# Performance work log

Hardware: AMD Instinct MI355X
Metric: run time of the kernel (lower is better)

Reference implementation:

```python
import jax, jax.numpy as jnp
import numpy as np

N = 64      # SSM state size (hidden_size)
H = 1024    # channels
L = 2048    # sequence length
BATCH = 8


def setup_inputs() -> dict:
    key = jax.random.key(0)
    ks = jax.random.split(key, 12)
    s = 1.0 / np.sqrt(N)
    n = jnp.arange(N, dtype=jnp.float32)
    return {
        "r": jax.random.normal(ks[0], (BATCH, L, H), dtype=jnp.float32),
        "B_re": jax.random.normal(ks[1], (N,), dtype=jnp.float32) * s,
        "B_im": jax.random.normal(ks[2], (N,), dtype=jnp.float32) * s,
        "C_re": jax.random.normal(ks[3], (H, N), dtype=jnp.float32) * s,
        "C_im": jax.random.normal(ks[4], (H, N), dtype=jnp.float32) * s,
        "P_re": jax.random.normal(ks[5], (N,), dtype=jnp.float32) * s,
        "P_im": jax.random.normal(ks[6], (N,), dtype=jnp.float32) * s,
        "Q_re": jax.random.normal(ks[7], (N,), dtype=jnp.float32) * s,
        "Q_im": jax.random.normal(ks[8], (N,), dtype=jnp.float32) * s,
        # HiPPO-LegS-like diagonal: negative real part for stability, imag ~ pi*n
        "diag_re": -0.5 * jnp.ones((N,), dtype=jnp.float32),
        "diag_im": jnp.pi * (n - N / 2.0),
        "step": jnp.array([1e-3], dtype=jnp.float32),
        "D": jnp.zeros((1,), dtype=jnp.float32),
    }


def _dplr_kernel(Bc, Cc, Pc, Qc, Lam, step, seq_len):
    # Standard S4 DPLR generating function evaluated at roots of unity,
    # then inverse FFT -> real convolution kernel K_c of shape (H, L).
    z = jnp.exp(-2j * jnp.pi * jnp.arange(seq_len) / seq_len).astype(jnp.complex64)  # (L,)
    g = (2.0 / step) * (1.0 - z) / (1.0 + z)                                          # (L,)
    cden = 1.0 / (g[:, None] - Lam[None, :])                                          # (L,N) Cauchy denom
    k00 = jnp.einsum('hn,ln->hl', Cc * Bc, cden)   # (H,L)
    k01 = jnp.einsum('hn,ln->hl', Cc * Pc, cden)   # (H,L)
    k10 = jnp.einsum('n,ln->l', Qc * Bc, cden)     # (L,)
    k11 = jnp.einsum('n,ln->l', Qc * Pc, cden)     # (L,)
    at_roots = (2.0 / (1.0 + z)) * (k00 - k01 * (k10 / (1.0 + k11)))  # (H,L)
    return jnp.fft.ifft(at_roots, axis=-1).real


def reference(r, B_re, B_im, C_re, C_im, P_re, P_im, Q_re, Q_im,
              diag_re, diag_im, step, D):
    step_c = jnp.maximum(step[0], 1e-6)
    Bc = B_re + 1j * B_im
    Cc = C_re + 1j * C_im
    Pc = P_re + 1j * P_im
    Qc = Q_re + 1j * Q_im
    Lam = diag_re + 1j * diag_im
    seq_len = r.shape[1]
    K = _dplr_kernel(Bc, Cc, Pc, Qc, Lam, step_c, seq_len)  # (H, L)
    # causal FFT convolution along the sequence axis
    nfft = 2 * seq_len
    Kf = jnp.fft.rfft(K, n=nfft, axis=-1)            # (H, nfft//2+1)
    uf = jnp.fft.rfft(r, n=nfft, axis=1)             # (B, nfft//2+1, H)
    h1 = jnp.fft.irfft(uf * Kf.T[None], n=nfft, axis=1)[:, :seq_len]  # (B,L,H)
    y1 = h1 + D[0] * r
    return jax.nn.gelu(y1, approximate=False)
```

## Files before the change

kernel.cpp:

```cpp
#include <hip/hip_runtime.h>
#include <math.h>

#define SSM_N 64
#define SSM_H 1024
#define SSM_L 2048
#define SSM_B 8
#define FFTN 2048
#define NT 256
#define NT2 512

#define PSWZ(a) ((a) ^ (((a) >> 4) & 15))

typedef float f2 __attribute__((ext_vector_type(2)));
static __device__ __forceinline__ f2 mkf2(float a, float b){ f2 v; v.x = a; v.y = b; return v; }

static __device__ __forceinline__ f2 cmul(f2 a, f2 b){
  return mkf2(-a.y, a.y) * mkf2(b.y, b.x) + mkf2(a.x, a.x) * b;
}
static __device__ __forceinline__ f2 cconj(f2 a){ return mkf2(a.x, -a.y); }

template<bool INV> static __device__ __forceinline__ f2 mul_mi(f2 a){
  return INV ? mkf2(-a.y, a.x) : mkf2(a.y, -a.x);
}
template<bool INV> static __device__ __forceinline__ f2 mul_w81(f2 a){
  const float r = 0.70710678118654752440f;
  return INV ? (r * mkf2(a.x - a.y, a.y + a.x)) : (r * mkf2(a.x + a.y, a.y - a.x));
}
template<bool INV> static __device__ __forceinline__ f2 mul_w83(f2 a){
  const float r = 0.70710678118654752440f;
  return INV ? (r * mkf2(-(a.x + a.y), a.x - a.y)) : (r * mkf2(a.y - a.x, -(a.x + a.y)));
}

#define W8C0 1.f
#define W8S0 0.f
#define W8C1 0.92387953251f
#define W8S1 (-0.38268343236f)
#define W8C2 0.70710678119f
#define W8S2 (-0.70710678119f)
#define W8C3 0.38268343236f
#define W8S3 (-0.92387953251f)
#define W8C4 0.f
#define W8S4 (-1.f)
#define W8C5 (-0.38268343236f)
#define W8S5 (-0.92387953251f)
#define W8C6 (-0.70710678119f)
#define W8S6 (-0.70710678119f)
#define W8C7 (-0.92387953251f)
#define W8S7 (-0.38268343236f)

template<bool INV>
static __device__ __forceinline__ void bfly8(const f2* x, f2* y)
{
  f2 t0=x[0]+x[4], t4=x[0]-x[4];
  f2 t1=x[1]+x[5], t5=x[1]-x[5];
  f2 t2=x[2]+x[6], t6=x[2]-x[6];
  f2 t3=x[3]+x[7], t7=x[3]-x[7];
  f2 b0=t0+t2, b2=t0-t2, b1=t1+t3, b3=t1-t3;
  f2 mb3 = mul_mi<INV>(b3);
  y[0]=b0+b1; y[4]=b0-b1; y[2]=b2+mb3; y[6]=b2-mb3;
  f2 v1 = mul_w81<INV>(t5), v2 = mul_mi<INV>(t6), v3 = mul_w83<INV>(t7);
  f2 a0=t4+v2, a2=t4-v2, a1=v1+v3, a3=v1-v3;
  f2 ma3 = mul_mi<INV>(a3);
  y[1]=a0+a1; y[5]=a0-a1; y[3]=a2+ma3; y[7]=a2-ma3;
}

template<bool INV>
static __device__ __forceinline__ void calc_w8(const f2* __restrict__ tw, int j, f2* w)
{
  f2 w1 = tw[j];
  if (INV) w1.y = -w1.y;
  w[1]=w1; w[2]=cmul(w1,w1); w[3]=cmul(w[2],w1); w[4]=cmul(w[2],w[2]);
  w[5]=cmul(w[3],w[2]); w[6]=cmul(w[3],w[3]); w[7]=cmul(w[4],w[3]);
}

static __device__ __forceinline__ void twstore(f2* __restrict__ dst, const f2* y, const f2* w,
                                               int base, int S)
{
  dst[PSWZ(base)]     = y[0];
  dst[PSWZ(base+S)]   = cmul(y[1],w[1]);
  dst[PSWZ(base+2*S)] = cmul(y[2],w[2]);
  dst[PSWZ(base+3*S)] = cmul(y[3],w[3]);
  dst[PSWZ(base+4*S)] = cmul(y[4],w[4]);
  dst[PSWZ(base+5*S)] = cmul(y[5],w[5]);
  dst[PSWZ(base+6*S)] = cmul(y[6],w[6]);
  dst[PSWZ(base+7*S)] = cmul(y[7],w[7]);
}

template<bool INV>
static __device__ __forceinline__ void bfly8_store(f2* __restrict__ dst, const f2* __restrict__ tw,
                                                   f2* x, int j, int base, int S)
{
  f2 y[8]; bfly8<INV>(x, y);
  f2 w[8]; calc_w8<INV>(tw, j, w);
  twstore(dst, y, w, base, S);
}

template<bool INV, bool ZTOP>
static __device__ __forceinline__ void stage8_first(const f2* __restrict__ src, f2* __restrict__ dst,
                                                    const f2* __restrict__ tw, int t, int st)
{
  const f2* sp = src + st;
  f2 x[8];
  if (ZTOP) {
    #pragma unroll
    for (int q = 0; q < 4; ++q) { x[q] = sp[256*q]; x[q+4] = mkf2(0.f, 0.f); }
  } else {
    #pragma unroll
    for (int q = 0; q < 8; ++q) x[q] = sp[256*q];
  }
  bfly8_store<INV>(dst, tw, x, t, t*8, 1);
}

template<bool INV, int S>
static __device__ __forceinline__ void stage8_mid(const f2* __restrict__ src, f2* __restrict__ dst,
                                                  const f2* __restrict__ tw, int t, int st)
{
  const f2* sp = src + st;
  f2 x[8];
  #pragma unroll
  for (int q = 0; q < 8; ++q) x[q] = sp[256*q];
  int i = t & (S-1);
  int j = t - i;
  bfly8_store<INV>(dst, tw, x, j, i + j*8, S);
}

template<bool INV, int S>
static __device__ __forceinline__ void stage8_mid_ip(f2* __restrict__ buf, const f2* __restrict__ tw,
                                                     int t, int st)
{
  f2 x[8];
  #pragma unroll
  for (int q = 0; q < 8; ++q) x[q] = buf[st + 256*q];
  __syncthreads();
  int i = t & (S-1);
  int j = t - i;
  bfly8_store<INV>(buf, tw, x, j, i + j*8, S);
  __syncthreads();
}

template<bool INV, bool HALFOUT>
static __device__ __forceinline__ void stage4f(const f2* __restrict__ src, f2* __restrict__ dst, int st)
{
  #pragma unroll
  for (int hh = 0; hh < 2; ++hh) {
    const f2* sp = src + st + 256*hh;
    f2* wp = dst + st + 256*hh;
    f2 x0=sp[0], x1=sp[512], x2=sp[1024], x3=sp[1536];
    f2 a0=x0+x2, a2=x0-x2, a1=x1+x3, a3=x1-x3;
    f2 m = mul_mi<INV>(a3);
    wp[0]   = a0+a1;
    wp[512] = a2+m;
    if (!HALFOUT) {
      wp[1024] = a0-a1;
      wp[1536] = a2-m;
    }
  }
}

template<bool INV>
static __device__ __forceinline__ void stage4f_ip(f2* __restrict__ buf, int st)
{
  f2 xr[2][4];
  #pragma unroll
  for (int hh = 0; hh < 2; ++hh) {
    const f2* sp = buf + st + 256*hh;
    xr[hh][0]=sp[0]; xr[hh][1]=sp[512]; xr[hh][2]=sp[1024]; xr[hh][3]=sp[1536];
  }
  __syncthreads();
  #pragma unroll
  for (int hh = 0; hh < 2; ++hh) {
    f2* wp = buf + st + 256*hh;
    f2 a0=xr[hh][0]+xr[hh][2], a2=xr[hh][0]-xr[hh][2];
    f2 a1=xr[hh][1]+xr[hh][3], a3=xr[hh][1]-xr[hh][3];
    f2 m = mul_mi<INV>(a3);
    wp[0]    = a0+a1;
    wp[512]  = a2+m;
    wp[1024] = a0-a1;
    wp[1536] = a2-m;
  }
  __syncthreads();
}

template<bool INV>
static __device__ __forceinline__ void stage4f_reg(const f2* __restrict__ src, f2* out, int st)
{
  #pragma unroll
  for (int hh = 0; hh < 2; ++hh) {
    const f2* sp = src + st + 256*hh;
    f2 x0=sp[0], x1=sp[512], x2=sp[1024], x3=sp[1536];
    f2 a0=x0+x2, a2=x0-x2, a1=x1+x3, a3=x1-x3;
    f2 m = mul_mi<INV>(a3);
    out[hh]   = a0+a1;
    out[hh+2] = a2+m;
    out[hh+4] = a0-a1;
    out[hh+6] = a2-m;
  }
}

static __device__ __forceinline__ f2 init_tw(f2* tw, int t)
{
  float s, c;
  sincosf(-6.2831853071795864769f * (float)t / (float)FFTN, &s, &c);
  f2 v = mkf2(c, s);
  tw[t] = v;
  return v;
}

__global__ __launch_bounds__(256) void kprep(
    const float* __restrict__ B_re, const float* __restrict__ B_im,
    const float* __restrict__ P_re, const float* __restrict__ P_im,
    const float* __restrict__ Q_re, const float* __restrict__ Q_im,
    const float* __restrict__ diag_re, const float* __restrict__ diag_im,
    const float* __restrict__ step,
    f2* __restrict__ cdenT, f2* __restrict__ f2v, f2* __restrict__ facv)
{
  int gid = blockIdx.x * 256 + threadIdx.x;
  int l = gid >> 3, s = gid & 7;
  double stepc = (double)step[0]; if (stepc < 1e-6) stepc = 1e-6;
  double ang = -2.0 * 3.14159265358979323846 * (double)l / (double)SSM_L;
  double zr = cos(ang), zi = sin(ang);
  double dr = 1.0 + zr, di = zi;
  double nr = 1.0 - zr, ni = -zi;
  double den = dr*dr + di*di;
  double i2s = 2.0 / stepc;
  double gr = i2s * (nr*dr + ni*di) / den;
  double gi = i2s * (ni*dr - nr*di) / den;
  double k10r=0.0, k10i=0.0, k11r=0.0, k11i=0.0;
  #pragma unroll
  for (int q = 0; q < 8; ++q) {
    int n = s*8 + q;
    double ar = gr - (double)diag_re[n];
    double ai = gi - (double)diag_im[n];
    double d2 = ar*ar + ai*ai;
    double cr = ar/d2, ci = -ai/d2;
    cdenT[n*SSM_L + l] = mkf2((float)cr, (float)ci);
    double qr = (double)Q_re[n], qi = (double)Q_im[n];
    double br = (double)B_re[n], bi = (double)B_im[n];
    double pr = (double)P_re[n], pi = (double)P_im[n];
    double qbr = qr*br - qi*bi, qbi = qr*bi + qi*br;
    double qpr = qr*pr - qi*pi, qpi = qr*pi + qi*pr;
    k10r += qbr*cr - qbi*ci; k10i += qbr*ci + qbi*cr;
    k11r += qpr*cr - qpi*ci; k11i += qpr*ci + qpi*cr;
  }
  #pragma unroll
  for (int off = 1; off < 8; off <<= 1) {
    k10r += __shfl_xor(k10r, off);
    k10i += __shfl_xor(k10i, off);
    k11r += __shfl_xor(k11r, off);
    k11i += __shfl_xor(k11i, off);
  }
  if (s == 0) {
    f2v[l] = mkf2((float)(2.0*dr/den), (float)(-2.0*di/den));
    double er = 1.0 + k11r, ei = k11i;
    double ed = er*er + ei*ei;
    facv[l] = mkf2((float)((k10r*er + k10i*ei)/ed), (float)((k10i*er - k10r*ei)/ed));
  }
}

__global__ __launch_bounds__(NT2, 4) void kkern(
    const float* __restrict__ C_re, const float* __restrict__ C_im,
    const float* __restrict__ B_re, const float* __restrict__ B_im,
    const float* __restrict__ P_re, const float* __restrict__ P_im,
    const f2* __restrict__ cdenT, const f2* __restrict__ f2v, const f2* __restrict__ facv,
    float4* __restrict__ PQg)
{
  __shared__ f2 bufA[2][FFTN];
  __shared__ f2 bufB[2][FFTN];
  __shared__ f2 tw[256];
  int t = threadIdx.x;
  int tt = t & 255, ch = t >> 8, stt = PSWZ(tt);
  int h0 = blockIdx.x * 2;
  if (t < 256) init_tw(tw, t);
  f2* cbs = bufA[0];
  if (t < 128) {
    int h = h0 + (t >> 6), n = t & 63;
    f2 cc = mkf2(C_re[h*SSM_N + n], C_im[h*SSM_N + n]);
    cbs[t]       = cmul(cc, mkf2(B_re[n], B_im[n]));
    cbs[128 + t] = cmul(cc, mkf2(P_re[n], P_im[n]));
  }
  __syncthreads();
  f2 k00[2][4], k01[2][4];
  #pragma unroll
  for (int h2 = 0; h2 < 2; ++h2)
    #pragma unroll
    for (int i = 0; i < 4; ++i) { k00[h2][i] = mkf2(0.f,0.f); k01[h2][i] = mkf2(0.f,0.f); }
  f2 cd[4];
  #pragma unroll
  for (int i = 0; i < 4; ++i) cd[i] = cdenT[t + i*NT2];
  for (int n = 0; n < SSM_N; ++n) {
    f2 cdn[4];
    #pragma unroll
    for (int i = 0; i < 4; ++i) cdn[i] = cdenT[((n+1)&63)*SSM_L + t + i*NT2];
    #pragma unroll
    for (int h2 = 0; h2 < 2; ++h2) {
      f2 cb = cbs[h2*64 + n], cp = cbs[128 + h2*64 + n];
      #pragma unroll
      for (int i = 0; i < 4; ++i) {
        k00[h2][i] = k00[h2][i] + cmul(cb, cd[i]);
        k01[h2][i] = k01[h2][i] + cmul(cp, cd[i]);
      }
    }
    #pragma unroll
    for (int i = 0; i < 4; ++i) cd[i] = cdn[i];
  }
  __syncthreads();
  #pragma unroll
  for (int h2 = 0; h2 < 2; ++h2)
    #pragma unroll
    for (int i = 0; i < 4; ++i) {
      int l = t + i*NT2;
      f2 fv = f2v[l], fc = facv[l];
      bufA[h2][PSWZ(l)] = cmul(fv, k00[h2][i] - cmul(k01[h2][i], fc));
    }
  __syncthreads();
  f2* A  = bufA[ch];
  f2* Bb = bufB[ch];
  f2 ebin[4], e2048 = mkf2(0.f, 0.f);
  #pragma unroll
  for (int i = 0; i < 4; ++i) {
    int m = tt + i*256;
    if (m == 0) {
      ebin[0] = mkf2(A[0].x, 0.f);
      e2048   = mkf2(A[PSWZ(FFTN/2)].x, 0.f);
    } else {
      ebin[i] = 0.5f * (A[PSWZ(m)] + cconj(A[PSWZ(FFTN - m)]));
    }
  }
  stage8_first<true, false>(A, Bb, tw, tt, stt);
  __syncthreads();
  stage8_mid<true, 8>(Bb, A, tw, tt, stt);
  __syncthreads();
  stage8_mid<true, 64>(A, Bb, tw, tt, stt);
  __syncthreads();
  {
    f2 kr[8];
    stage4f_reg<true>(Bb, kr, stt);
    float sbb, cbb;
    sincosf(-3.14159265358979f * (float)tt / (float)FFTN, &sbb, &cbb);
    f2 cbase = mkf2(cbb, sbb);
    const float Wc8[8] = {W8C0,W8C1,W8C2,W8C3,W8C4,W8C5,W8C6,W8C7};
    const float Ws8[8] = {W8S0,W8S1,W8S2,W8S3,W8S4,W8S5,W8S6,W8S7};
    const float scale = 1.0f / (float)FFTN;
    #pragma unroll
    for (int q = 0; q < 8; ++q) {
      f2 tq = cmul(cbase, mkf2(Wc8[q], Ws8[q]));
      kr[q] = (kr[q].x * scale) * tq;
    }
    f2 w[8]; calc_w8<false>(tw, tt, w);
    f2 y[8]; bfly8<false>(kr, y); twstore(A, y, w, tt*8, 1);
  }
  __syncthreads();
  stage8_mid<false, 8>(A, Bb, tw, tt, stt);
  __syncthreads();
  stage8_mid<false, 64>(Bb, A, tw, tt, stt);
  __syncthreads();
  stage4f<false, true>(A, Bb, stt);
  #pragma unroll
  for (int i = 0; i < 4; ++i) {
    int m = tt + 256*i;
    f2 v = ebin[i];
    if (m == 0) v = e2048;
    Bb[1024 + m] = v;
  }
  __syncthreads();
  f2 u = tw[tt];
  const float q4 = 1.0f / 4096.0f;
  const f2 c1 = mkf2(0.99999882345170176f, -0.00153398018628477f);
  f2 base_odd = cmul(c1, u);
  const float Wc8[8] = {W8C0,W8C1,W8C2,W8C3,W8C4,W8C5,W8C6,W8C7};
  const float Ws8[8] = {W8S0,W8S1,W8S2,W8S3,W8S4,W8S5,W8S6,W8S7};
  float4* pqrow = PQg + (size_t)(h0 + ch) * FFTN;
  #pragma unroll
  for (int i = 0; i < 4; ++i) {
    int m = tt + 256*i;
    f2 Ka = ebin[i];
    f2 Kb = Bb[1024 + ((1024 - m) & 1023)];
    f2 ee = cmul(u, mkf2(Wc8[2*i], Ws8[2*i]));
    float cv = ee.x, sv = -ee.y;
    float am = q4*(1.f - sv), ap = q4*(1.f + sv), cq = q4*cv;
    f2 P = mkf2(Ka.x*am + Kb.x*ap, Ka.y*am - Kb.y*ap);
    f2 dd = mkf2(Ka.x - Kb.x, Ka.y + Kb.y);
    pqrow[2*m] = make_float4(P.x, P.y, -dd.y*cq, dd.x*cq);
    f2 Ko = Bb[PSWZ(m)];
    f2 Kp = Bb[PSWZ(1023 - m)];
    f2 eo = cmul(base_odd, mkf2(Wc8[2*i], Ws8[2*i]));
    cv = eo.x; sv = -eo.y;
    am = q4*(1.f - sv); ap = q4*(1.f + sv); cq = q4*cv;
    f2 P2 = mkf2(Ko.x*am + Kp.x*ap, Ko.y*am - Kp.y*ap);
    f2 d2 = mkf2(Ko.x - Kp.x, Ko.y + Kp.y);
    pqrow[2*m+1] = make_float4(P2.x, P2.y, -d2.y*cq, d2.x*cq);
  }
}

__global__ __launch_bounds__(NT, 4) void kconv(const float* __restrict__ r,
                                               const float4* __restrict__ PQg,
                                               const float* __restrict__ Dp,
                                               float* __restrict__ out)
{
  __shared__ f2 buf[FFTN];
  __shared__ f2 tw[256];
  int t = threadIdx.x, st = PSWZ(t);
  int xcd = blockIdx.x & 7, local = blockIdx.x >> 3;
  int h = (xcd << 7) | (local & 127);
  int b = local >> 7;
  float Dv = Dp[0];
  const float* rp = r + (size_t)b * SSM_L * SSM_H + h;
  f2 rv[4];
  #pragma unroll
  for (int i = 0; i < 4; ++i) {
    int j2 = t + i*NT;
    rv[i] = mkf2(rp[(size_t)(2*j2) * SSM_H], rp[(size_t)(2*j2 + 1) * SSM_H]);
  }
  init_tw(tw, t);
  {
    f2 xx[8];
    #pragma unroll
    for (int q = 0; q < 4; ++q) { xx[q] = rv[q]; xx[q+4] = mkf2(0.f, 0.f); }
    bfly8_store<false>(buf, tw, xx, t, t*8, 1);
  }
  __syncthreads();
  stage8_mid_ip<false, 8>(buf, tw, t, st);
  stage8_mid_ip<false, 64>(buf, tw, t, st);
  const float4* pqrow = PQg + (size_t)h * FFTN;
  float4 pq[8];
  #pragma unroll
  for (int i = 0; i < 8; ++i) pq[i] = pqrow[t + i*NT];
  stage4f_ip<false>(buf, st);
  {
    f2 xx[8];
    #pragma unroll
    for (int i = 0; i < 8; ++i) {
      int k = t + i*NT;
      int kk = (FFTN - k) & (FFTN - 1);
      f2 Ck  = buf[st + i*NT];
      f2 Ckk = buf[PSWZ(kk)];
      xx[i] = cmul(mkf2(pq[i].x, pq[i].y), Ck) + cmul(mkf2(pq[i].z, pq[i].w), cconj(Ckk));
    }
    __syncthreads();
    bfly8_store<true>(buf, tw, xx, t, t*8, 1);
  }
  __syncthreads();
  stage8_mid_ip<true, 8>(buf, tw, t, st);
  stage8_mid_ip<true, 64>(buf, tw, t, st);
  float* op = out + (size_t)b * SSM_L * SSM_H + h;
  const float kq = 0.70710678118654752f;
  #pragma unroll
  for (int hh = 0; hh < 2; ++hh) {
    const f2* sp = buf + st + 256*hh;
    f2 x0=sp[0], x1=sp[512], x2=sp[1024], x3=sp[1536];
    f2 a0=x0+x2, a2=x0-x2, a1=x1+x3, a3=x1-x3;
    f2 mm = mul_mi<true>(a3);
    f2 y0 = a0+a1, y1 = a2+mm;
    f2 rA = rv[hh], rB = rv[hh+2];
    int j0 = t + 256*hh, j1 = t + 256*hh + 512;
    float v0 = y0.x + Dv*rA.x, v1 = y0.y + Dv*rA.y;
    float v2 = y1.x + Dv*rB.x, v3 = y1.y + Dv*rB.y;
    op[(size_t)(2*j0    ) * SSM_H] = 0.5f * v0 * (1.0f + erff(v0 * kq));
    op[(size_t)(2*j0 + 1) * SSM_H] = 0.5f * v1 * (1.0f + erff(v1 * kq));
    op[(size_t)(2*j1    ) * SSM_H] = 0.5f * v2 * (1.0f + erff(v2 * kq));
    op[(size_t)(2*j1 + 1) * SSM_H] = 0.5f * v3 * (1.0f + erff(v3 * kq));
  }
}

extern "C" void kernel_launch(void* const* d_in, const int* in_sizes, int n_in,
                              void* d_out, int out_size, void* d_ws, size_t ws_size,
                              hipStream_t stream)
{
  const float* r       = (const float*)d_in[0];
  const float* B_re    = (const float*)d_in[1];
  const float* B_im    = (const float*)d_in[2];
  const float* C_re    = (const float*)d_in[3];
  const float* C_im    = (const float*)d_in[4];
  const float* P_re    = (const float*)d_in[5];
  const float* P_im    = (const float*)d_in[6];
  const float* Q_re    = (const float*)d_in[7];
  const float* Q_im    = (const float*)d_in[8];
  const float* diag_re = (const float*)d_in[9];
  const float* diag_im = (const float*)d_in[10];
  const float* step    = (const float*)d_in[11];
  const float* Dp      = (const float*)d_in[12];
  float* out = (float*)d_out;

  char* p = (char*)d_ws;
  f2* cdenT  = (f2*)p;     p += (size_t)SSM_N*SSM_L*sizeof(f2);
  f2* f2v    = (f2*)p;     p += (size_t)SSM_L*sizeof(f2);
  f2* facv   = (f2*)p;     p += (size_t)SSM_L*sizeof(f2);
  float4* PQ = (float4*)p; p += (size_t)SSM_H*FFTN*sizeof(float4);

  kprep<<<64, 256, 0, stream>>>(B_re, B_im, P_re, P_im, Q_re, Q_im,
                                diag_re, diag_im, step, cdenT, f2v, facv);
  kkern<<<SSM_H/2, NT2, 0, stream>>>(C_re, C_im, B_re, B_im, P_re, P_im,
                                     cdenT, f2v, facv, PQ);
  kconv<<<SSM_B*SSM_H, NT, 0, stream>>>(r, PQ, Dp, out);
}
```

Measured before the change: 305.1 us.

## Pre-transpose input to channel-major layout in prep kernel for coalesced conv loads

Adds a tiled shared-memory transpose of r (B,L,H) to a workspace rT of shape (B,H,L), run by the first 4096 blocks of the prep kernel alongside the original DPLR precompute blocks. The convolution kernel then reads each channel's sequence contiguously as f2 pairs instead of making strided gathers with stride H. This removes uncoalesced reads in kconv at the cost of an extra full read and write pass over the 64 MB input.

```diff
diff --git a/kernel.cpp b/kernel.cpp
--- a/kernel.cpp
+++ b/kernel.cpp
@@ -207,6 +207,7 @@
 }
 
 __global__ __launch_bounds__(256) void kprep(
+    const float* __restrict__ r, float* __restrict__ rT,
     const float* __restrict__ B_re, const float* __restrict__ B_im,
     const float* __restrict__ P_re, const float* __restrict__ P_im,
     const float* __restrict__ Q_re, const float* __restrict__ Q_im,
@@ -214,46 +215,71 @@
     const float* __restrict__ step,
     f2* __restrict__ cdenT, f2* __restrict__ f2v, f2* __restrict__ facv)
 {
-  int gid = blockIdx.x * 256 + threadIdx.x;
-  int l = gid >> 3, s = gid & 7;
-  double stepc = (double)step[0]; if (stepc < 1e-6) stepc = 1e-6;
-  double ang = -2.0 * 3.14159265358979323846 * (double)l / (double)SSM_L;
-  double zr = cos(ang), zi = sin(ang);
-  double dr = 1.0 + zr, di = zi;
-  double nr = 1.0 - zr, ni = -zi;
-  double den = dr*dr + di*di;
-  double i2s = 2.0 / stepc;
-  double gr = i2s * (nr*dr + ni*di) / den;
-  double gi = i2s * (ni*dr - nr*di) / den;
-  double k10r=0.0, k10i=0.0, k11r=0.0, k11i=0.0;
-  #pragma unroll
-  for (int q = 0; q < 8; ++q) {
-    int n = s*8 + q;
-    double ar = gr - (double)diag_re[n];
-    double ai = gi - (double)diag_im[n];
-    double d2 = ar*ar + ai*ai;
-    double cr = ar/d2, ci = -ai/d2;
-    cdenT[n*SSM_L + l] = mkf2((float)cr, (float)ci);
-    double qr = (double)Q_re[n], qi = (double)Q_im[n];
-    double br = (double)B_re[n], bi = (double)B_im[n];
-    double pr = (double)P_re[n], pi = (double)P_im[n];
-    double qbr = qr*br - qi*bi, qbi = qr*bi + qi*br;
-    double qpr = qr*pr - qi*pi, qpi = qr*pi + qi*pr;
-    k10r += qbr*cr - qbi*ci; k10i += qbr*ci + qbi*cr;
-    k11r += qpr*cr - qpi*ci; k11i += qpr*ci + qpi*cr;
-  }
-  #pragma unroll
-  for (int off = 1; off < 8; off <<= 1) {
-    k10r += __shfl_xor(k10r, off);
-    k10i += __shfl_xor(k10i, off);
-    k11r += __shfl_xor(k11r, off);
-    k11i += __shfl_xor(k11i, off);
-  }
-  if (s == 0) {
-    f2v[l] = mkf2((float)(2.0*dr/den), (float)(-2.0*di/den));
-    double er = 1.0 + k11r, ei = k11i;
-    double ed = er*er + ei*ei;
-    facv[l] = mkf2((float)((k10r*er + k10i*ei)/ed), (float)((k10i*er - k10r*ei)/ed));
+  __shared__ float til[64][65];
+  int bid = blockIdx.x;
+  int t = threadIdx.x;
+  if (bid < 4096) {
+    int tx = t & 15, ty = t >> 4;
+    int h0 = (bid & 15) * 64, l0 = ((bid >> 4) & 31) * 64, b = bid >> 9;
+    const float4* s4 = (const float4*)(r + ((size_t)b*SSM_L + l0)*SSM_H + h0);
+    #pragma unroll
+    for (int i = 0; i < 4; ++i) {
+      int lr = ty + 16*i;
+      float4 v = s4[(size_t)lr*(SSM_H/4) + tx];
+      til[lr][4*tx+0]=v.x; til[lr][4*tx+1]=v.y; til[lr][4*tx+2]=v.z; til[lr][4*tx+3]=v.w;
+    }
+    __syncthreads();
+    float4* d4 = (float4*)(rT + ((size_t)b*SSM_H + h0)*SSM_L + l0);
+    #pragma unroll
+    for (int i = 0; i < 4; ++i) {
+      int hr = ty + 16*i;
+      float4 w;
+      w.x = til[4*tx+0][hr]; w.y = til[4*tx+1][hr];
+      w.z = til[4*tx+2][hr]; w.w = til[4*tx+3][hr];
+      d4[(size_t)hr*(SSM_L/4) + tx] = w;
+    }
+  } else {
+    int gid = (bid - 4096) * 256 + t;
+    int l = gid >> 3, s = gid & 7;
+    double stepc = (double)step[0]; if (stepc < 1e-6) stepc = 1e-6;
+    double ang = -2.0 * 3.14159265358979323846 * (double)l / (double)SSM_L;
+    double zr = cos(ang), zi = sin(ang);
+    double dr = 1.0 + zr, di = zi;
+    double nr = 1.0 - zr, ni = -zi;
+    double den = dr*dr + di*di;
+    double i2s = 2.0 / stepc;
+    double gr = i2s * (nr*dr + ni*di) / den;
+    double gi = i2s * (ni*dr - nr*di) / den;
+    double k10r=0.0, k10i=0.0, k11r=0.0, k11i=0.0;
+    #pragma unroll
+    for (int q = 0; q < 8; ++q) {
+      int n = s*8 + q;
+      double ar = gr - (double)diag_re[n];
+      double ai = gi - (double)diag_im[n];
+      double d2 = ar*ar + ai*ai;
+      double cr = ar/d2, ci = -ai/d2;
+      cdenT[n*SSM_L + l] = mkf2((float)cr, (float)ci);
+      double qr = (double)Q_re[n], qi = (double)Q_im[n];
+      double br = (double)B_re[n], bi = (double)B_im[n];
+      double pr = (double)P_re[n], pi = (double)P_im[n];
+      double qbr = qr*br - qi*bi, qbi = qr*bi + qi*br;
+      double qpr = qr*pr - qi*pi, qpi = qr*pi + qi*pr;
+      k10r += qbr*cr - qbi*ci; k10i += qbr*ci + qbi*cr;
+      k11r += qpr*cr - qpi*ci; k11i += qpr*ci + qpi*cr;
+    }
+    #pragma unroll
+    for (int off = 1; off < 8; off <<= 1) {
+      k10r += __shfl_xor(k10r, off);
+      k10i += __shfl_xor(k10i, off);
+      k11r += __shfl_xor(k11r, off);
+      k11i += __shfl_xor(k11i, off);
+    }
+    if (s == 0) {
+      f2v[l] = mkf2((float)(2.0*dr/den), (float)(-2.0*di/den));
+      double er = 1.0 + k11r, ei = k11i;
+      double ed = er*er + ei*ei;
+      facv[l] = mkf2((float)((k10r*er + k10i*ei)/ed), (float)((k10i*er - k10r*ei)/ed));
+    }
   }
 }
 
@@ -392,7 +418,7 @@
   }
 }
 
-__global__ __launch_bounds__(NT, 4) void kconv(const float* __restrict__ r,
+__global__ __launch_bounds__(NT, 4) void kconv(const float* __restrict__ rT,
                                                const float4* __restrict__ PQg,
                                                const float* __restrict__ Dp,
                                                float* __restrict__ out)
@@ -404,14 +430,11 @@
   int h = (xcd << 7) | (local & 127);
   int b = local >> 7;
   float Dv = Dp[0];
-  const float* rp = r + (size_t)b * SSM_L * SSM_H + h;
+  init_tw(tw, t);
+  const f2* r2 = (const f2*)(rT + ((size_t)b*SSM_H + h) * SSM_L);
   f2 rv[4];
   #pragma unroll
-  for (int i = 0; i < 4; ++i) {
-    int j2 = t + i*NT;
-    rv[i] = mkf2(rp[(size_t)(2*j2) * SSM_H], rp[(size_t)(2*j2 + 1) * SSM_H]);
-  }
-  init_tw(tw, t);
+  for (int i = 0; i < 4; ++i) rv[i] = r2[t + i*NT];
   {
     f2 xx[8];
     #pragma unroll
@@ -482,14 +505,15 @@
   float* out = (float*)d_out;
 
   char* p = (char*)d_ws;
+  float* rT  = (float*)p;  p += (size_t)SSM_B*SSM_H*SSM_L*sizeof(float);
   f2* cdenT  = (f2*)p;     p += (size_t)SSM_N*SSM_L*sizeof(f2);
   f2* f2v    = (f2*)p;     p += (size_t)SSM_L*sizeof(f2);
   f2* facv   = (f2*)p;     p += (size_t)SSM_L*sizeof(f2);
   float4* PQ = (float4*)p; p += (size_t)SSM_H*FFTN*sizeof(float4);
 
-  kprep<<<64, 256, 0, stream>>>(B_re, B_im, P_re, P_im, Q_re, Q_im,
-                                diag_re, diag_im, step, cdenT, f2v, facv);
+  kprep<<<4096 + 64, 256, 0, stream>>>(r, rT, B_re, B_im, P_re, P_im, Q_re, Q_im,
+                                       diag_re, diag_im, step, cdenT, f2v, facv);
   kkern<<<SSM_H/2, NT2, 0, stream>>>(C_re, C_im, B_re, B_im, P_re, P_im,
                                      cdenT, f2v, facv, PQ);
-  kconv<<<SSM_B*SSM_H, NT, 0, stream>>>(r, PQ, Dp, out);
-}
+  kconv<<<SSM_B*SSM_H, NT, 0, stream>>>(rT, PQ, Dp, out);
+}
```

After: 282.8 us. 1.08x faster.
